# Optimization experiments

Measured on AMD Instinct MI355X. Metric: run time of the kernel, lower is better.

## Reference

```python
import jax, jax.numpy as jnp
import numpy as np

N_FEATURE = 12
SIGMA = 0.015
NODES = jnp.linspace(0.0, 0.3, 12)  # RBF centers, matches torch.linspace(0,0.3,12)

B, N, K, FIN = 16, 4096, 32, 4


def setup_inputs() -> dict:
    key = jax.random.key(0)
    ks = jax.random.split(key, 24)

    def make_d(ki, kd):
        idx = jax.random.randint(ki, (B, N, K), 0, N).astype(jnp.float32)
        dist = jax.random.uniform(kd, (B, N, K), minval=0.0, maxval=0.3)
        return jnp.stack([idx, dist], axis=-1)  # [B,N,K,2]

    def lin(kw, kb, fin, fout):
        W = jax.random.normal(kw, (fin, fout), jnp.float32) * (1.0 / np.sqrt(fin))
        b = jax.random.normal(kb, (fout,), jnp.float32) * 0.01
        return W, b

    x = jax.random.normal(ks[0], (B, N, FIN), jnp.float32)
    d1 = make_d(ks[1], ks[2])
    d0 = make_d(ks[3], ks[4])
    dm1 = make_d(ks[5], ks[6])
    mask = jnp.ones((B, N), dtype=bool)

    We, be = lin(ks[7], ks[8], FIN, N_FEATURE)
    Wm1, bm1 = lin(ks[9], ks[10], N_FEATURE + 12, N_FEATURE)
    Wu1, bu1 = lin(ks[11], ks[12], 2 * N_FEATURE, N_FEATURE)
    Wm0, bm0 = lin(ks[13], ks[14], N_FEATURE + 12, N_FEATURE)
    Wu0, bu0 = lin(ks[15], ks[16], 2 * N_FEATURE, N_FEATURE)
    Wmm1, bmm1 = lin(ks[17], ks[18], N_FEATURE + 12, N_FEATURE)
    Wum1, bum1 = lin(ks[19], ks[20], 2 * N_FEATURE, N_FEATURE)

    return {"x": x, "d1": d1, "d0": d0, "dm1": dm1, "mask": mask,
            "We": We, "be": be, "Wm1": Wm1, "bm1": bm1, "Wu1": Wu1, "bu1": bu1,
            "Wm0": Wm0, "bm0": bm0, "Wu0": Wu0, "bu0": bu0,
            "Wmm1": Wmm1, "bmm1": bmm1, "Wum1": Wum1, "bum1": bum1}


def _branch(h, d, Wm, bm, Wu, bu):
    # d: [B,N,K,2] -> channel 0 neighbor index, channel 1 distance
    idx = d[..., 0].astype(jnp.int32)                     # [B,N,K]
    rbf = jnp.exp(-((d[..., 1][..., None] - NODES) ** 2) / (2.0 * SIGMA ** 2))  # [B,N,K,12]
    hj = jax.vmap(lambda hb, ib: hb[ib])(h, idx)          # gather: [B,N,K,F]
    hd = jnp.concatenate([hj, rbf], axis=-1)              # [B,N,K,F+12]
    m = jax.nn.relu(hd @ Wm + bm).sum(axis=2)             # [B,N,F]
    return jax.nn.sigmoid(jnp.concatenate([h, m], axis=-1) @ Wu + bu)  # [B,N,F]


def reference(x, d1, d0, dm1, mask,
              We, be, Wm1, bm1, Wu1, bu1,
              Wm0, bm0, Wu0, bu0,
              Wmm1, bmm1, Wum1, bum1):
    h = jax.nn.relu(x @ We + be)                          # [B,N,12]
    h1 = _branch(h, d1, Wm1, bm1, Wu1, bu1)
    h0 = _branch(h, d0, Wm0, bm0, Wu0, bu0)
    hm1 = _branch(h, dm1, Wmm1, bmm1, Wum1, bum1)
    return (h1, h0, hm1)
```

## Files before the change

### kernel.cpp

```cpp
#include <hip/hip_runtime.h>
#include <hip/hip_fp16.h>
#include <math.h>

#define BBAT 16
#define NNODE 4096
#define KNB 32
#define NF 12
#define TBL 512
#define NPB 820
#define TMAIN 832

#define LDS_BYTES 110616

__device__ __forceinline__ __half2 u2h(unsigned int u) { __half2 h; __builtin_memcpy(&h, &u, 4); return h; }
__device__ __forceinline__ unsigned int h2u(__half2 h) { unsigned int u; __builtin_memcpy(&u, &h, 4); return u; }
__device__ __forceinline__ float4 ldf4(const float* p) { return *(const float4*)p; }

__global__ __launch_bounds__(TMAIN) void fused_kernel(
    const float* __restrict__ x, const float* __restrict__ We, const float* __restrict__ be,
    const float* __restrict__ Wm1, const float* __restrict__ bm1,
    const float* __restrict__ Wm0, const float* __restrict__ bm0,
    const float* __restrict__ Wmm1, const float* __restrict__ bmm1,
    const float* __restrict__ d1, const float* __restrict__ d0, const float* __restrict__ dm1,
    const float* __restrict__ Wu1, const float* __restrict__ bu1,
    const float* __restrict__ Wu0, const float* __restrict__ bu0,
    const float* __restrict__ Wum1, const float* __restrict__ bum1,
    float* __restrict__ out)
{
    extern __shared__ char smem[];
    uint4* gAl = (uint4*)smem;
    uint2* gBl = (uint2*)(smem + 65536);
    uint4* tAl = (uint4*)(smem + 98304);
    uint2* tBl = (uint2*)(smem + 106512);

    const int q = blockIdx.x, b = blockIdx.y, br = blockIdx.z;
    const int tid = threadIdx.x;
    const size_t slice = (size_t)(br * BBAT + b) * NNODE;

    const float* Wm = (br == 0) ? Wm1 : (br == 1) ? Wm0 : Wmm1;
    const float* bm = (br == 0) ? bm1 : (br == 1) ? bm0 : bmm1;

    if (tid <= TBL) {
        float dd = (float)tid * (0.3f / (float)TBL);
        float rbf[12];
#pragma unroll
        for (int j = 0; j < 12; j++) {
            float t = dd - (0.3f / 11.0f) * (float)j;
            rbf[j] = expf(-2222.2222222222f * t * t);
        }
        float ph[NF];
#pragma unroll
        for (int c = 0; c < NF; c++) {
            float s = 0.0f;
#pragma unroll
            for (int j = 0; j < 12; j++) s = fmaf(rbf[j], Wm[(12 + j) * NF + c], s);
            ph[c] = s;
        }
        uint4 a; uint2 bv;
        a.x  = h2u(__floats2half2_rn(ph[0],  ph[1]));
        a.y  = h2u(__floats2half2_rn(ph[2],  ph[3]));
        a.z  = h2u(__floats2half2_rn(ph[4],  ph[5]));
        a.w  = h2u(__floats2half2_rn(ph[6],  ph[7]));
        bv.x = h2u(__floats2half2_rn(ph[8],  ph[9]));
        bv.y = h2u(__floats2half2_rn(ph[10], ph[11]));
        tAl[tid] = a;
        tBl[tid] = bv;
    }

    for (int i = tid; i < NNODE; i += TMAIN) {
        float4 xv = ((const float4*)x)[(size_t)b * NNODE + i];
        float hv[NF];
#pragma unroll
        for (int f = 0; f < NF; f++) {
            float s = be[f];
            s = fmaf(xv.x, We[0 * NF + f], s);
            s = fmaf(xv.y, We[1 * NF + f], s);
            s = fmaf(xv.z, We[2 * NF + f], s);
            s = fmaf(xv.w, We[3 * NF + f], s);
            hv[f] = fmaxf(s, 0.0f);
        }
        float g[NF];
#pragma unroll
        for (int c = 0; c < NF; c++) {
            float s = bm[c];
#pragma unroll
            for (int j = 0; j < NF; j++) s = fmaf(hv[j], Wm[j * NF + c], s);
            g[c] = s;
        }
        uint4 a; uint2 bv;
        a.x  = h2u(__floats2half2_rn(g[0],  g[1]));
        a.y  = h2u(__floats2half2_rn(g[2],  g[3]));
        a.z  = h2u(__floats2half2_rn(g[4],  g[5]));
        a.w  = h2u(__floats2half2_rn(g[6],  g[7]));
        bv.x = h2u(__floats2half2_rn(g[8],  g[9]));
        bv.y = h2u(__floats2half2_rn(g[10], g[11]));
        gAl[i] = a;
        gBl[i] = bv;
    }
    __syncthreads();

    const int n = q * NPB + tid;
    if (tid >= NPB || n >= NNODE) return;

    const float* dsel = (br == 0) ? d1 : (br == 1) ? d0 : dm1;
    const float* Wu   = (br == 0) ? Wu1 : (br == 1) ? Wu0 : Wum1;
    const float* bu   = (br == 0) ? bu1 : (br == 1) ? bu0 : bum1;

    float m[NF];
#pragma unroll
    for (int f = 0; f < NF; f++) m[f] = 0.0f;

    const float4* dp = (const float4*)(dsel + ((size_t)b * NNODE + n) * (size_t)(KNB * 2));

#define ACC(O, G, T0, T1) {                                                    \
        __half2 t0 = u2h(T0), t1 = u2h(T1);                                    \
        __half2 phi = __hfma2(f2, __hsub2(t1, t0), t0);                        \
        __half2 s2 = __hadd2(u2h(G), phi);                                     \
        float2 sf = __half22float2(s2);                                        \
        m[O]     += fmaxf(sf.x, 0.0f);                                         \
        m[O + 1] += fmaxf(sf.y, 0.0f);                                         \
    }

#pragma unroll
    for (int kt = 0; kt < 4; kt++) {
        float4 e0 = dp[kt * 4 + 0];
        float4 e1 = dp[kt * 4 + 1];
        float4 e2 = dp[kt * 4 + 2];
        float4 e3 = dp[kt * 4 + 3];
        float idxf[8] = { e0.x, e0.z, e1.x, e1.z, e2.x, e2.z, e3.x, e3.z };
        float dist[8] = { e0.y, e0.w, e1.y, e1.w, e2.y, e2.w, e3.y, e3.w };
#pragma unroll
        for (int ee = 0; ee < 8; ee++) {
            int j = (int)idxf[ee];
            uint4 ga = gAl[j];
            uint2 gb = gBl[j];
            float uu = dist[ee] * ((float)TBL / 0.3f);
            int i = (int)uu;
            i = min(i, TBL - 1);
            float fr = uu - (float)i;
            __half2 f2 = __float2half2_rn(fr);
            uint4 a0 = tAl[i];
            uint2 b0 = tBl[i];
            uint4 a1 = tAl[i + 1];
            uint2 b1 = tBl[i + 1];
            ACC(0,  ga.x, a0.x, a1.x)
            ACC(2,  ga.y, a0.y, a1.y)
            ACC(4,  ga.z, a0.z, a1.z)
            ACC(6,  ga.w, a0.w, a1.w)
            ACC(8,  gb.x, b0.x, b1.x)
            ACC(10, gb.y, b0.y, b1.y)
        }
    }
#undef ACC

    float4 xv = ((const float4*)x)[(size_t)b * NNODE + n];
    float hv[NF];
#pragma unroll
    for (int f = 0; f < NF; f++) {
        float s = be[f];
        s = fmaf(xv.x, We[0 * NF + f], s);
        s = fmaf(xv.y, We[1 * NF + f], s);
        s = fmaf(xv.z, We[2 * NF + f], s);
        s = fmaf(xv.w, We[3 * NF + f], s);
        hv[f] = fmaxf(s, 0.0f);
    }

    float ov[NF];
#pragma unroll
    for (int f = 0; f < NF; f++) {
        float a = bu[f];
#pragma unroll
        for (int j = 0; j < NF; j++) a = fmaf(hv[j], Wu[j * NF + f], a);
#pragma unroll
        for (int j = 0; j < NF; j++) a = fmaf(m[j], Wu[(NF + j) * NF + f], a);
        ov[f] = 1.0f / (1.0f + __expf(-a));
    }
    float* op = out + (slice + n) * NF;
    ((float4*)op)[0] = make_float4(ov[0], ov[1], ov[2],  ov[3]);
    ((float4*)op)[1] = make_float4(ov[4], ov[5], ov[6],  ov[7]);
    ((float4*)op)[2] = make_float4(ov[8], ov[9], ov[10], ov[11]);
}

extern "C" void kernel_launch(void* const* d_in, const int* in_sizes, int n_in,
                              void* d_out, int out_size, void* d_ws, size_t ws_size,
                              hipStream_t stream)
{
    const float* x    = (const float*)d_in[0];
    const float* d1   = (const float*)d_in[1];
    const float* d0   = (const float*)d_in[2];
    const float* dm1  = (const float*)d_in[3];
    const float* We   = (const float*)d_in[5];
    const float* be   = (const float*)d_in[6];
    const float* Wm1  = (const float*)d_in[7];
    const float* bm1  = (const float*)d_in[8];
    const float* Wu1  = (const float*)d_in[9];
    const float* bu1  = (const float*)d_in[10];
    const float* Wm0  = (const float*)d_in[11];
    const float* bm0  = (const float*)d_in[12];
    const float* Wu0  = (const float*)d_in[13];
    const float* bu0  = (const float*)d_in[14];
    const float* Wmm1 = (const float*)d_in[15];
    const float* bmm1 = (const float*)d_in[16];
    const float* Wum1 = (const float*)d_in[17];
    const float* bum1 = (const float*)d_in[18];

    hipFuncSetAttribute((const void*)fused_kernel,
                        hipFuncAttributeMaxDynamicSharedMemorySize, LDS_BYTES);

    fused_kernel<<<dim3(5, BBAT, 3), TMAIN, LDS_BYTES, stream>>>(
        x, We, be, Wm1, bm1, Wm0, bm0, Wmm1, bmm1,
        d1, d0, dm1, Wu1, bu1, Wu0, bu0, Wum1, bum1, (float*)d_out);
}
```

Measured before the change: 150.9 us.

## Split each node's edges across four lanes with shuffle reduction and split LDS tables

Each node's 32 edges are now handled by 4 threads (8 edges each), reduced with xor shuffles, and the final update layer is split so each lane writes 3 outputs. The grid grows from 5 to 16 chunks per batch/branch with 1024-thread blocks. The gather and RBF tables move to six planar uint2 arrays, with a pre-shifted copy of the table for the interpolation neighbour, and the edge data is loaded before the barrier while the next gather is prefetched. This is meant to raise parallelism and hide latency, but each block now rebuilds the full 4096-node G table for only 256 nodes, which multiplies the redundant prologue work.

```diff
diff --git a/kernel.cpp b/kernel.cpp
--- a/kernel.cpp
+++ b/kernel.cpp
@@ -7,14 +7,14 @@
 #define KNB 32
 #define NF 12
 #define TBL 512
-#define NPB 820
-#define TMAIN 832
-
-#define LDS_BYTES 110616
+#define TMAIN 1024
+#define NPB 256
+#define CHUNKS 16
+
+#define LDS_BYTES 122880
 
 __device__ __forceinline__ __half2 u2h(unsigned int u) { __half2 h; __builtin_memcpy(&h, &u, 4); return h; }
 __device__ __forceinline__ unsigned int h2u(__half2 h) { unsigned int u; __builtin_memcpy(&u, &h, 4); return u; }
-__device__ __forceinline__ float4 ldf4(const float* p) { return *(const float4*)p; }
 
 __global__ __launch_bounds__(TMAIN) void fused_kernel(
     const float* __restrict__ x, const float* __restrict__ We, const float* __restrict__ be,
@@ -28,17 +28,28 @@
     float* __restrict__ out)
 {
     extern __shared__ char smem[];
-    uint4* gAl = (uint4*)smem;
-    uint2* gBl = (uint2*)(smem + 65536);
-    uint4* tAl = (uint4*)(smem + 98304);
-    uint2* tBl = (uint2*)(smem + 106512);
+    uint2* G0l = (uint2*)smem;
+    uint2* G1l = (uint2*)(smem + 32768);
+    uint2* G2l = (uint2*)(smem + 65536);
+    uint2* A0l = (uint2*)(smem + 98304);
+    uint2* A1l = (uint2*)(smem + 102400);
+    uint2* A2l = (uint2*)(smem + 106496);
+    uint2* A3l = (uint2*)(smem + 110592);
+    uint2* A4l = (uint2*)(smem + 114688);
+    uint2* A5l = (uint2*)(smem + 118784);
 
     const int q = blockIdx.x, b = blockIdx.y, br = blockIdx.z;
     const int tid = threadIdx.x;
+    const int nl = tid >> 2, sub = tid & 3;
+    const int n = q * NPB + nl;
     const size_t slice = (size_t)(br * BBAT + b) * NNODE;
 
     const float* Wm = (br == 0) ? Wm1 : (br == 1) ? Wm0 : Wmm1;
     const float* bm = (br == 0) ? bm1 : (br == 1) ? bm0 : bmm1;
+    const float* dsel = (br == 0) ? d1 : (br == 1) ? d0 : dm1;
+
+    const float4* dp = (const float4*)(dsel + ((size_t)b * NNODE + n) * (size_t)(KNB * 2)) + sub * 4;
+    float4 dr0 = dp[0], dr1 = dp[1], dr2 = dp[2], dr3 = dp[3];
 
     if (tid <= TBL) {
         float dd = (float)tid * (0.3f / (float)TBL);
@@ -56,18 +67,27 @@
             for (int j = 0; j < 12; j++) s = fmaf(rbf[j], Wm[(12 + j) * NF + c], s);
             ph[c] = s;
         }
-        uint4 a; uint2 bv;
-        a.x  = h2u(__floats2half2_rn(ph[0],  ph[1]));
-        a.y  = h2u(__floats2half2_rn(ph[2],  ph[3]));
-        a.z  = h2u(__floats2half2_rn(ph[4],  ph[5]));
-        a.w  = h2u(__floats2half2_rn(ph[6],  ph[7]));
-        bv.x = h2u(__floats2half2_rn(ph[8],  ph[9]));
-        bv.y = h2u(__floats2half2_rn(ph[10], ph[11]));
-        tAl[tid] = a;
-        tBl[tid] = bv;
-    }
-
-    for (int i = tid; i < NNODE; i += TMAIN) {
+        unsigned int c0 = h2u(__floats2half2_rn(ph[0],  ph[1]));
+        unsigned int c1 = h2u(__floats2half2_rn(ph[2],  ph[3]));
+        unsigned int c2 = h2u(__floats2half2_rn(ph[4],  ph[5]));
+        unsigned int c3 = h2u(__floats2half2_rn(ph[6],  ph[7]));
+        unsigned int c4 = h2u(__floats2half2_rn(ph[8],  ph[9]));
+        unsigned int c5 = h2u(__floats2half2_rn(ph[10], ph[11]));
+        if (tid < TBL) {
+            A0l[tid] = make_uint2(c0, c1);
+            A1l[tid] = make_uint2(c2, c3);
+            A2l[tid] = make_uint2(c4, c5);
+        }
+        if (tid >= 1) {
+            A3l[tid - 1] = make_uint2(c0, c1);
+            A4l[tid - 1] = make_uint2(c2, c3);
+            A5l[tid - 1] = make_uint2(c4, c5);
+        }
+    }
+
+#pragma unroll
+    for (int it = 0; it < 4; it++) {
+        const int i = it * TMAIN + tid;
         float4 xv = ((const float4*)x)[(size_t)b * NNODE + i];
         float hv[NF];
 #pragma unroll
@@ -87,30 +107,26 @@
             for (int j = 0; j < NF; j++) s = fmaf(hv[j], Wm[j * NF + c], s);
             g[c] = s;
         }
-        uint4 a; uint2 bv;
-        a.x  = h2u(__floats2half2_rn(g[0],  g[1]));
-        a.y  = h2u(__floats2half2_rn(g[2],  g[3]));
-        a.z  = h2u(__floats2half2_rn(g[4],  g[5]));
-        a.w  = h2u(__floats2half2_rn(g[6],  g[7]));
-        bv.x = h2u(__floats2half2_rn(g[8],  g[9]));
-        bv.y = h2u(__floats2half2_rn(g[10], g[11]));
-        gAl[i] = a;
-        gBl[i] = bv;
+        G0l[i] = make_uint2(h2u(__floats2half2_rn(g[0], g[1])),  h2u(__floats2half2_rn(g[2],  g[3])));
+        G1l[i] = make_uint2(h2u(__floats2half2_rn(g[4], g[5])),  h2u(__floats2half2_rn(g[6],  g[7])));
+        G2l[i] = make_uint2(h2u(__floats2half2_rn(g[8], g[9])),  h2u(__floats2half2_rn(g[10], g[11])));
     }
     __syncthreads();
 
-    const int n = q * NPB + tid;
-    if (tid >= NPB || n >= NNODE) return;
-
-    const float* dsel = (br == 0) ? d1 : (br == 1) ? d0 : dm1;
-    const float* Wu   = (br == 0) ? Wu1 : (br == 1) ? Wu0 : Wum1;
-    const float* bu   = (br == 0) ? bu1 : (br == 1) ? bu0 : bum1;
+    int   jv[8];
+    float uv[8];
+    jv[0] = (int)dr0.x; uv[0] = dr0.y * ((float)TBL / 0.3f);
+    jv[1] = (int)dr0.z; uv[1] = dr0.w * ((float)TBL / 0.3f);
+    jv[2] = (int)dr1.x; uv[2] = dr1.y * ((float)TBL / 0.3f);
+    jv[3] = (int)dr1.z; uv[3] = dr1.w * ((float)TBL / 0.3f);
+    jv[4] = (int)dr2.x; uv[4] = dr2.y * ((float)TBL / 0.3f);
+    jv[5] = (int)dr2.z; uv[5] = dr2.w * ((float)TBL / 0.3f);
+    jv[6] = (int)dr3.x; uv[6] = dr3.y * ((float)TBL / 0.3f);
+    jv[7] = (int)dr3.z; uv[7] = dr3.w * ((float)TBL / 0.3f);
 
     float m[NF];
 #pragma unroll
     for (int f = 0; f < NF; f++) m[f] = 0.0f;
-
-    const float4* dp = (const float4*)(dsel + ((size_t)b * NNODE + n) * (size_t)(KNB * 2));
 
 #define ACC(O, G, T0, T1) {                                                    \
         __half2 t0 = u2h(T0), t1 = u2h(T1);                                    \
@@ -121,37 +137,46 @@
         m[O + 1] += fmaxf(sf.y, 0.0f);                                         \
     }
 
-#pragma unroll
-    for (int kt = 0; kt < 4; kt++) {
-        float4 e0 = dp[kt * 4 + 0];
-        float4 e1 = dp[kt * 4 + 1];
-        float4 e2 = dp[kt * 4 + 2];
-        float4 e3 = dp[kt * 4 + 3];
-        float idxf[8] = { e0.x, e0.z, e1.x, e1.z, e2.x, e2.z, e3.x, e3.z };
-        float dist[8] = { e0.y, e0.w, e1.y, e1.w, e2.y, e2.w, e3.y, e3.w };
-#pragma unroll
-        for (int ee = 0; ee < 8; ee++) {
-            int j = (int)idxf[ee];
-            uint4 ga = gAl[j];
-            uint2 gb = gBl[j];
-            float uu = dist[ee] * ((float)TBL / 0.3f);
-            int i = (int)uu;
-            i = min(i, TBL - 1);
-            float fr = uu - (float)i;
-            __half2 f2 = __float2half2_rn(fr);
-            uint4 a0 = tAl[i];
-            uint2 b0 = tBl[i];
-            uint4 a1 = tAl[i + 1];
-            uint2 b1 = tBl[i + 1];
-            ACC(0,  ga.x, a0.x, a1.x)
-            ACC(2,  ga.y, a0.y, a1.y)
-            ACC(4,  ga.z, a0.z, a1.z)
-            ACC(6,  ga.w, a0.w, a1.w)
-            ACC(8,  gb.x, b0.x, b1.x)
-            ACC(10, gb.y, b0.y, b1.y)
-        }
-    }
+#define EDGE(GC0, GC1, GC2, GN0, GN1, GN2, E, PREF)                            \
+    {                                                                          \
+        if (PREF) { int jn = jv[(E) + 1];                                      \
+            GN0 = G0l[jn]; GN1 = G1l[jn]; GN2 = G2l[jn]; }                     \
+        float uu = uv[E];                                                      \
+        int ii = (int)uu;                                                      \
+        ii = min(ii, TBL - 1);                                                 \
+        float fr = uu - (float)ii;                                             \
+        __half2 f2 = __float2half2_rn(fr);                                     \
+        uint2 a0 = A0l[ii], a1 = A1l[ii], a2 = A2l[ii];                        \
+        uint2 a3 = A3l[ii], a4 = A4l[ii], a5 = A5l[ii];                        \
+        ACC(0,  GC0.x, a0.x, a3.x)                                             \
+        ACC(2,  GC0.y, a0.y, a3.y)                                             \
+        ACC(4,  GC1.x, a1.x, a4.x)                                             \
+        ACC(6,  GC1.y, a1.y, a4.y)                                             \
+        ACC(8,  GC2.x, a2.x, a5.x)                                             \
+        ACC(10, GC2.y, a2.y, a5.y)                                             \
+    }
+
+    uint2 pa0, pa1, pa2, pb0, pb1, pb2;
+    { int j0 = jv[0]; pa0 = G0l[j0]; pa1 = G1l[j0]; pa2 = G2l[j0]; }
+    EDGE(pa0, pa1, pa2, pb0, pb1, pb2, 0, 1)
+    EDGE(pb0, pb1, pb2, pa0, pa1, pa2, 1, 1)
+    EDGE(pa0, pa1, pa2, pb0, pb1, pb2, 2, 1)
+    EDGE(pb0, pb1, pb2, pa0, pa1, pa2, 3, 1)
+    EDGE(pa0, pa1, pa2, pb0, pb1, pb2, 4, 1)
+    EDGE(pb0, pb1, pb2, pa0, pa1, pa2, 5, 1)
+    EDGE(pa0, pa1, pa2, pb0, pb1, pb2, 6, 1)
+    EDGE(pb0, pb1, pb2, pa0, pa1, pa2, 7, 0)
+
+#undef EDGE
 #undef ACC
+
+#pragma unroll
+    for (int f = 0; f < NF; f++) m[f] += __shfl_xor(m[f], 1);
+#pragma unroll
+    for (int f = 0; f < NF; f++) m[f] += __shfl_xor(m[f], 2);
+
+    const float* Wu = (br == 0) ? Wu1 : (br == 1) ? Wu0 : Wum1;
+    const float* bu = (br == 0) ? bu1 : (br == 1) ? bu0 : bum1;
 
     float4 xv = ((const float4*)x)[(size_t)b * NNODE + n];
     float hv[NF];
@@ -165,20 +190,18 @@
         hv[f] = fmaxf(s, 0.0f);
     }
 
-    float ov[NF];
-#pragma unroll
-    for (int f = 0; f < NF; f++) {
+    const int f0 = sub * 3;
+    float* op = out + (slice + n) * NF + f0;
+#pragma unroll
+    for (int ff = 0; ff < 3; ff++) {
+        const int f = f0 + ff;
         float a = bu[f];
 #pragma unroll
         for (int j = 0; j < NF; j++) a = fmaf(hv[j], Wu[j * NF + f], a);
 #pragma unroll
         for (int j = 0; j < NF; j++) a = fmaf(m[j], Wu[(NF + j) * NF + f], a);
-        ov[f] = 1.0f / (1.0f + __expf(-a));
-    }
-    float* op = out + (slice + n) * NF;
-    ((float4*)op)[0] = make_float4(ov[0], ov[1], ov[2],  ov[3]);
-    ((float4*)op)[1] = make_float4(ov[4], ov[5], ov[6],  ov[7]);
-    ((float4*)op)[2] = make_float4(ov[8], ov[9], ov[10], ov[11]);
+        op[ff] = 1.0f / (1.0f + __expf(-a));
+    }
 }
 
 extern "C" void kernel_launch(void* const* d_in, const int* in_sizes, int n_in,
@@ -207,7 +230,7 @@
     hipFuncSetAttribute((const void*)fused_kernel,
                         hipFuncAttributeMaxDynamicSharedMemorySize, LDS_BYTES);
 
-    fused_kernel<<<dim3(5, BBAT, 3), TMAIN, LDS_BYTES, stream>>>(
+    fused_kernel<<<dim3(CHUNKS, BBAT, 3), TMAIN, LDS_BYTES, stream>>>(
         x, We, be, Wm1, bm1, Wm0, bm0, Wmm1, bmm1,
         d1, d0, dm1, Wu1, bu1, Wu0, bu0, Wum1, bum1, (float*)d_out);
 }
```

Measured after the change: 172.6 us. 1.14x slower.
